# Kernel tuning notes

Measured on AMD Instinct MI355X. Metric: run time of the kernel, lower is better.

## Reference

```python
import jax, jax.numpy as jnp
import numpy as np
import math

EMBED_DIM = 256
N_HEAD = 8
N_LEVELS = 4
N_POINTS = 4
HEAD_DIM = EMBED_DIM // N_HEAD
TOTAL_POINTS = N_HEAD * N_LEVELS * N_POINTS
SPATIAL = np.array([[100, 100], [50, 50], [25, 25], [13, 13]], dtype=np.int32)
BS = 2
LEN_Q = int(SPATIAL.prod(1).sum())  # 13294, encoder self-attention
LEN_V = LEN_Q


def setup_inputs() -> dict:
    key = jax.random.key(0)
    ks = jax.random.split(key, 12)
    s = 1.0 / math.sqrt(EMBED_DIM)
    inp = {
        'query': jax.random.normal(ks[0], (BS, LEN_Q, EMBED_DIM), jnp.float32),
        'reference_points': jax.random.uniform(ks[1], (BS, LEN_Q, N_LEVELS, 2), jnp.float32),
        'value': jax.random.normal(ks[2], (BS, LEN_V, EMBED_DIM), jnp.float32),
        'value_spatial_shapes': jnp.asarray(SPATIAL),
        'W_value': jax.random.normal(ks[3], (EMBED_DIM, EMBED_DIM), jnp.float32) * s,
        'b_value': jnp.zeros((EMBED_DIM,), jnp.float32),
        'W_off': jax.random.normal(ks[4], (TOTAL_POINTS * 2, EMBED_DIM), jnp.float32) * 0.01,
        'b_off': jax.random.normal(ks[5], (TOTAL_POINTS * 2,), jnp.float32),
        'W_attn': jax.random.normal(ks[6], (TOTAL_POINTS, EMBED_DIM), jnp.float32) * s,
        'b_attn': jnp.zeros((TOTAL_POINTS,), jnp.float32),
        'W_out': jax.random.normal(ks[7], (EMBED_DIM, EMBED_DIM), jnp.float32) * s,
        'b_out': jnp.zeros((EMBED_DIM,), jnp.float32),
        'zeta': jnp.ones((1, 1, 1, HEAD_DIM), jnp.float32),  # search_type='embed'
    }
    return inp


def _grid_sample_bilinear(img, gx, gy):
    """img: [B,H,W,c]; gx,gy: [B,Q,P] normalized to [-1,1].
    align_corners=False, padding_mode='zeros' (matches F.grid_sample)."""
    B, H, W, c = img.shape
    x = (gx + 1.0) * (0.5 * W) - 0.5
    y = (gy + 1.0) * (0.5 * H) - 0.5
    x0 = jnp.floor(x)
    y0 = jnp.floor(y)
    wx = (x - x0)[..., None]
    wy = (y - y0)[..., None]
    flat = img.reshape(B, H * W, c)

    def gather(xi, yi):
        m = (xi >= 0) & (xi < W) & (yi >= 0) & (yi < H)
        xi_c = jnp.clip(xi, 0, W - 1).astype(jnp.int32)
        yi_c = jnp.clip(yi, 0, H - 1).astype(jnp.int32)
        idx = (yi_c * W + xi_c).reshape(B, -1, 1)
        v = jnp.take_along_axis(flat, idx, axis=1).reshape(B, *xi.shape[1:], c)
        return v * m[..., None]

    v00 = gather(x0, y0)
    v01 = gather(x0 + 1, y0)
    v10 = gather(x0, y0 + 1)
    v11 = gather(x0 + 1, y0 + 1)
    return (v00 * (1 - wx) * (1 - wy) + v01 * wx * (1 - wy)
            + v10 * (1 - wx) * wy + v11 * wx * wy)


def reference(query, reference_points, value, value_spatial_shapes,
              W_value, b_value, W_off, b_off, W_attn, b_attn, W_out, b_out, zeta):
    bs, Len_q, _ = query.shape
    Len_v = value.shape[1]
    shapes = np.asarray(value_spatial_shapes)  # static ints

    # value projection + sparse gate (zeta, not pruned/searched)
    v = value @ W_value.T + b_value
    v = v.reshape(bs, Len_v, N_HEAD, HEAD_DIM) * zeta  # [bs,Lv,h,c]

    # sampling offsets and attention weights from query
    off = (query @ W_off.T + b_off).reshape(bs, Len_q, N_HEAD, N_LEVELS, N_POINTS, 2)
    attn = (query @ W_attn.T + b_attn).reshape(bs, Len_q, N_HEAD, N_LEVELS * N_POINTS)
    attn = jax.nn.softmax(attn, axis=-1).reshape(bs, Len_q, N_HEAD, N_LEVELS, N_POINTS)

    # reference_points last dim == 2 branch
    normalizer = jnp.asarray(shapes[:, ::-1], jnp.float32).reshape(1, 1, 1, N_LEVELS, 1, 2)  # (W,H)
    loc = reference_points.reshape(bs, Len_q, 1, N_LEVELS, 1, 2) + off / normalizer
    grids = 2.0 * loc - 1.0  # [bs,Lq,h,L,P,2]

    B = bs * N_HEAD
    out = jnp.zeros((B, Len_q, HEAD_DIM), jnp.float32)
    start = 0
    for lvl in range(N_LEVELS):
        h, w = int(shapes[lvl, 0]), int(shapes[lvl, 1])
        # [bs, h*w, nh, c] -> [bs*nh, h, w, c]
        v_l = v[:, start:start + h * w].transpose(0, 2, 1, 3).reshape(B, h, w, HEAD_DIM)
        g = grids[:, :, :, lvl].transpose(0, 2, 1, 3, 4).reshape(B, Len_q, N_POINTS, 2)
        samp = _grid_sample_bilinear(v_l, g[..., 0], g[..., 1])  # [B,Lq,P,c]
        a_l = attn[:, :, :, lvl].transpose(0, 2, 1, 3).reshape(B, Len_q, N_POINTS)
        out = out + jnp.einsum('bqpc,bqp->bqc', samp, a_l)
        start += h * w

    out = out.reshape(bs, N_HEAD, Len_q, HEAD_DIM).transpose(0, 2, 1, 3).reshape(bs, Len_q, EMBED_DIM)
    return out @ W_out.T + b_out
```

## Files before the change

kernel.cpp:

```cpp
#include <hip/hip_runtime.h>


#define LQ    13294
#define NTOK  26588
#define NE    6806528

typedef unsigned short ushort_t;
typedef __attribute__((ext_vector_type(8))) short short8;
typedef __attribute__((ext_vector_type(4))) float float4_t;
typedef __attribute__((ext_vector_type(2))) unsigned int uint2_t;

__device__ __forceinline__ ushort_t f2b(float f) {
    unsigned int x = __float_as_uint(f);
    return (ushort_t)((x + 0x7fffu + ((x >> 16) & 1u)) >> 16);
}

__device__ __forceinline__ void gload16(const void* g, void* l) {
    __builtin_amdgcn_global_load_lds(
        (const __attribute__((address_space(1))) unsigned int*)g,
        (__attribute__((address_space(3))) unsigned int*)l, 16, 0, 0);
}

__device__ __forceinline__ void cvt_seg(const float* __restrict__ s,
                                        ushort_t* __restrict__ d,
                                        int n4, int gid, int stride) {
    const float4_t* s4 = (const float4_t*)s;
    for (int i = gid; i < n4; i += stride) {
        float4_t f = s4[i];
        ushort4 o;
        o.x = f2b(f.x); o.y = f2b(f.y); o.z = f2b(f.z); o.w = f2b(f.w);
        *(ushort4*)(d + (long)i * 4) = o;
    }
}

__global__ __launch_bounds__(256) void cvt_k(
    const float* q, const float* v, const float* Wv, const float* Wo,
    const float* Wa, const float* Wout,
    ushort_t* q_bf, ushort_t* v_bf, ushort_t* Wv_bf, ushort_t* WoWa_bf,
    ushort_t* Wout_bf)
{
    const int gid = blockIdx.x * 256 + threadIdx.x;
    const int stride = gridDim.x * 256;
    cvt_seg(q,    q_bf,            NE / 4,     gid, stride);
    cvt_seg(v,    v_bf,            NE / 4,     gid, stride);
    cvt_seg(Wv,   Wv_bf,           65536 / 4,  gid, stride);
    cvt_seg(Wo,   WoWa_bf,         65536 / 4,  gid, stride);
    cvt_seg(Wa,   WoWa_bf + 65536, 32768 / 4,  gid, stride);
    cvt_seg(Wout, Wout_bf,         65536 / 4,  gid, stride);
}

__device__ __forceinline__ void gemm_tile(
    const ushort_t* __restrict__ A,
    const ushort_t* __restrict__ W,
    int m0, int n0,
    ushort_t* As, ushort_t* Bs, float4_t acc[2][4])
{
    const int tid = threadIdx.x;
    const int w  = tid >> 6;
    const int ln = tid & 63;
    const int lr = ln >> 2;
    const int lc = (ln & 3) * 8;

    ushort_t* lA0 = As + (w * 2 + 0) * 512;
    ushort_t* lA1 = As + (w * 2 + 1) * 512;
    ushort_t* lB  = Bs + w * 512;
    const ushort_t* gA0 = A + (long)(m0 + w * 32 + lr) * 256 + lc;
    const ushort_t* gA1 = gA0 + 16 * 256;
    const ushort_t* gB  = W + (long)(n0 + w * 16 + lr) * 256 + lc;

    const int krow = (ln >> 4) * 8;
    const int fr   = ln & 15;

    for (int k0 = 0; k0 < 256; k0 += 32) {
        gload16(gA0 + k0, lA0);
        gload16(gA1 + k0, lA1);
        gload16(gB  + k0, lB);
        __syncthreads();

        short8 af[2], bfr[4];
        #pragma unroll
        for (int i = 0; i < 2; i++)
            af[i] = *(const short8*)(As + (w * 32 + i * 16 + fr) * 32 + krow);
        #pragma unroll
        for (int j = 0; j < 4; j++)
            bfr[j] = *(const short8*)(Bs + (j * 16 + fr) * 32 + krow);
        #pragma unroll
        for (int i = 0; i < 2; i++)
            #pragma unroll
            for (int j = 0; j < 4; j++)
                acc[i][j] = __builtin_amdgcn_mfma_f32_16x16x32_bf16(af[i], bfr[j], acc[i][j], 0, 0, 0);
        __syncthreads();
    }
}

__global__ __launch_bounds__(256) void gemm_fused_k(
    const ushort_t* __restrict__ q_bf, const ushort_t* __restrict__ v_bf,
    const ushort_t* __restrict__ Wv,   const ushort_t* __restrict__ WoWa,
    const float* __restrict__ b_value, const float* __restrict__ b_off,
    const float* __restrict__ b_attn,  const float* __restrict__ zeta,
    ushort_t* __restrict__ vproj, float* __restrict__ oa)
{
    __shared__ __align__(16) ushort_t As[128 * 32];
    __shared__ __align__(16) ushort_t Bs[64 * 32];

    const int z = blockIdx.z;
    const int bid = blockIdx.x;
    int x, y;
    if (z == 0) {
        if (bid >= 832) return;
        int id = (bid & 7) * 104 + (bid >> 3);
        x = id >> 2; y = id & 3;
    } else {
        int id = (bid & 7) * 156 + (bid >> 3);
        x = id / 6; y = id - x * 6;
    }
    const int m0 = x * 128;
    const int n0 = y * 64;

    float4_t acc[2][4] = {};
    gemm_tile(z ? q_bf : v_bf, z ? WoWa : Wv, m0, n0, As, Bs, acc);

    const int tid = threadIdx.x;
    const int w = tid >> 6, ln = tid & 63;
    const int col = ln & 15;
    const int rq  = (ln >> 4) * 4;
    #pragma unroll
    for (int j = 0; j < 4; j++) {
        int n = n0 + j * 16 + col;
        if (z == 0) {
            float bz = b_value[n];
            float zz = zeta[n & 31];
            #pragma unroll
            for (int i = 0; i < 2; i++) {
                #pragma unroll
                for (int r = 0; r < 4; r++) {
                    int m = m0 + w * 32 + i * 16 + rq + r;
                    if (m < NTOK) vproj[(long)m * 256 + n] = f2b((acc[i][j][r] + bz) * zz);
                }
            }
        } else {
            float bz = (n < 256) ? b_off[n] : b_attn[n - 256];
            #pragma unroll
            for (int i = 0; i < 2; i++) {
                #pragma unroll
                for (int r = 0; r < 4; r++) {
                    int m = m0 + w * 32 + i * 16 + rq + r;
                    if (m < NTOK) oa[(long)m * 384 + n] = acc[i][j][r] + bz;
                }
            }
        }
    }
}

__global__ __launch_bounds__(256) void gemm_out_k(
    const ushort_t* __restrict__ A,
    const ushort_t* __restrict__ W,
    const float* __restrict__ bias,
    float* __restrict__ C)
{
    __shared__ __align__(16) ushort_t As[128 * 32];
    __shared__ __align__(16) ushort_t Bs[64 * 32];

    const int bid = blockIdx.x;
    int id = (bid & 7) * 104 + (bid >> 3);
    const int m0 = (id >> 2) * 128;
    const int n0 = (id & 3) * 64;

    float4_t acc[2][4] = {};
    gemm_tile(A, W, m0, n0, As, Bs, acc);

    const int tid = threadIdx.x;
    const int w = tid >> 6, ln = tid & 63;
    const int col = ln & 15;
    const int rq  = (ln >> 4) * 4;
    #pragma unroll
    for (int j = 0; j < 4; j++) {
        int n = n0 + j * 16 + col;
        float bz = bias[n];
        #pragma unroll
        for (int i = 0; i < 2; i++) {
            #pragma unroll
            for (int r = 0; r < 4; r++) {
                int m = m0 + w * 32 + i * 16 + rq + r;
                if (m < NTOK) C[(long)m * 256 + n] = acc[i][j][r] + bz;
            }
        }
    }
}

__global__ __launch_bounds__(512) void sample_k(
    const float* __restrict__ refp,
    const ushort_t* __restrict__ v,
    const float* __restrict__ oa,
    ushort_t* __restrict__ outp)
{
    __shared__ int   p_ofs[512][4];
    __shared__ float p_w[512][4];
    const int tid = threadIdx.x;
    const int t0 = blockIdx.x * 4;

    {
        const int tok = tid >> 7, wt = tid & 127;
        const long t = t0 + tok;
        const int h = wt >> 4, pi = wt & 15;
        const int lvl = pi >> 2;
        const int Wi  = (lvl == 0) ? 100 : (lvl == 1) ? 50 : (lvl == 2) ? 25 : 13;
        const int st  = (lvl == 0) ? 0 : (lvl == 1) ? 10000 : (lvl == 2) ? 12500 : 13125;
        const float Wf = (float)Wi;

        float lg = oa[t * 384 + 256 + h * 16 + pi];
        float smax = lg;
        #pragma unroll
        for (int d = 1; d < 16; d <<= 1) smax = fmaxf(smax, __shfl_xor(smax, d, 64));
        float ex = __expf(lg - smax);
        float sm = ex;
        #pragma unroll
        for (int d = 1; d < 16; d <<= 1) sm += __shfl_xor(sm, d, 64);
        const float a = ex / sm;

        float ox = oa[t * 384 + h * 32 + pi * 2];
        float oy = oa[t * 384 + h * 32 + pi * 2 + 1];
        float rx = refp[t * 8 + lvl * 2];
        float ry = refp[t * 8 + lvl * 2 + 1];

        float x = rx * Wf + ox - 0.5f;
        float y = ry * Wf + oy - 0.5f;
        float xf = floorf(x), yf = floorf(y);
        float wx = x - xf, wy = y - yf;
        int x0 = (int)xf, y0 = (int)yf;

        float mx0 = ((unsigned)x0       < (unsigned)Wi) ? (1.f - wx) : 0.f;
        float mx1 = ((unsigned)(x0 + 1) < (unsigned)Wi) ? wx         : 0.f;
        float my0 = ((unsigned)y0       < (unsigned)Wi) ? (1.f - wy) * a : 0.f;
        float my1 = ((unsigned)(y0 + 1) < (unsigned)Wi) ? wy * a         : 0.f;
        int x0c = min(max(x0, 0), Wi - 1);
        int x1c = min(max(x0 + 1, 0), Wi - 1);
        int y0c = min(max(y0, 0), Wi - 1);
        int y1c = min(max(y0 + 1, 0), Wi - 1);

        int r0 = st + y0c * Wi, r1 = st + y1c * Wi;
        p_ofs[tid][0] = (r0 + x0c) << 9;
        p_ofs[tid][1] = (r0 + x1c) << 9;
        p_ofs[tid][2] = (r1 + x0c) << 9;
        p_ofs[tid][3] = (r1 + x1c) << 9;
        p_w[tid][0] = mx0 * my0;
        p_w[tid][1] = mx1 * my0;
        p_w[tid][2] = mx0 * my1;
        p_w[tid][3] = mx1 * my1;
    }
    __syncthreads();

    const int tok = tid >> 7, wt = tid & 127;
    const long t = t0 + tok;
    const int b = (t >= LQ) ? 1 : 0;
    const int h = wt >> 4, s = (wt >> 3) & 1, g = wt & 7;
    const char* vb = (const char*)(v + ((long)b * LQ) * 256 + h * 32 + g * 4);
    const int base = tok * 128 + h * 16 + s * 8;
    float4_t acc = {0.f, 0.f, 0.f, 0.f};

    #pragma unroll 4
    for (int p = 0; p < 8; p++) {
        int4     o  = *(const int4*)p_ofs[base + p];
        float4_t w4 = *(const float4_t*)p_w[base + p];
        uint2_t u00 = *(const uint2_t*)(vb + o.x);
        uint2_t u01 = *(const uint2_t*)(vb + o.y);
        uint2_t u10 = *(const uint2_t*)(vb + o.z);
        uint2_t u11 = *(const uint2_t*)(vb + o.w);
        acc[0] += w4.x * __uint_as_float(u00.x << 16)
                + w4.y * __uint_as_float(u01.x << 16)
                + w4.z * __uint_as_float(u10.x << 16)
                + w4.w * __uint_as_float(u11.x << 16);
        acc[1] += w4.x * __uint_as_float(u00.x & 0xffff0000u)
                + w4.y * __uint_as_float(u01.x & 0xffff0000u)
                + w4.z * __uint_as_float(u10.x & 0xffff0000u)
                + w4.w * __uint_as_float(u11.x & 0xffff0000u);
        acc[2] += w4.x * __uint_as_float(u00.y << 16)
                + w4.y * __uint_as_float(u01.y << 16)
                + w4.z * __uint_as_float(u10.y << 16)
                + w4.w * __uint_as_float(u11.y << 16);
        acc[3] += w4.x * __uint_as_float(u00.y & 0xffff0000u)
                + w4.y * __uint_as_float(u01.y & 0xffff0000u)
                + w4.z * __uint_as_float(u10.y & 0xffff0000u)
                + w4.w * __uint_as_float(u11.y & 0xffff0000u);
    }

    acc.x += __shfl_down(acc.x, 8, 64);
    acc.y += __shfl_down(acc.y, 8, 64);
    acc.z += __shfl_down(acc.z, 8, 64);
    acc.w += __shfl_down(acc.w, 8, 64);

    if (s == 0) {
        ushort4 o;
        o.x = f2b(acc.x); o.y = f2b(acc.y); o.z = f2b(acc.z); o.w = f2b(acc.w);
        *(ushort4*)(outp + t * 256 + h * 32 + g * 4) = o;
    }
}

extern "C" void kernel_launch(void* const* d_in, const int* in_sizes, int n_in,
                              void* d_out, int out_size, void* d_ws, size_t ws_size,
                              hipStream_t stream)
{
    char* ws = (char*)d_ws;
    ushort_t* vproj   = (ushort_t*)ws;
    float*    oa      = (float*)(ws + (long)NE * 2);
    ushort_t* q_bf    = (ushort_t*)(ws + (long)NE * 2 + (long)NTOK * 1536);
    ushort_t* outpre  = q_bf;
    ushort_t* v_bf    = q_bf + NE;
    ushort_t* Wv_bf   = v_bf + NE;
    ushort_t* WoWa_bf = Wv_bf + 65536;
    ushort_t* Wout_bf = WoWa_bf + 98304;

    cvt_k<<<1024, 256, 0, stream>>>(
        (const float*)d_in[0], (const float*)d_in[2], (const float*)d_in[4],
        (const float*)d_in[6], (const float*)d_in[8], (const float*)d_in[10],
        q_bf, v_bf, Wv_bf, WoWa_bf, Wout_bf);

    gemm_fused_k<<<dim3(1248, 1, 2), 256, 0, stream>>>(
        q_bf, v_bf, Wv_bf, WoWa_bf,
        (const float*)d_in[5], (const float*)d_in[7], (const float*)d_in[9],
        (const float*)d_in[12], vproj, oa);

    sample_k<<<6647, 512, 0, stream>>>(
        (const float*)d_in[1], vproj, oa, outpre);

    gemm_out_k<<<832, 256, 0, stream>>>(
        outpre, Wout_bf, (const float*)d_in[11], (float*)d_out);
}
```

Baseline: 224.5 us.

## Head-major value layout, 16-byte gathers, and double-buffered GEMM tiles with preloaded weights

The value projection is now stored head-major ([head][token][32]), so each bilinear corner of one head is a contiguous 64-byte row. The sampler gathers 16 bytes per lane instead of 8, processes 8 tokens per block with padded shared-memory indexing, and halves the grid. The GEMM tile preloads the whole 64x256 weight slice into LDS and double-buffers the A tiles, which removes one barrier per k-step. In exchange, LDS per block grows substantially, which may reduce occupancy.

```diff
diff --git a/kernel.cpp b/kernel.cpp
--- a/kernel.cpp
+++ b/kernel.cpp
@@ -7,8 +7,8 @@
 
 typedef unsigned short ushort_t;
 typedef __attribute__((ext_vector_type(8))) short short8;
+typedef __attribute__((ext_vector_type(8))) unsigned short ushort8_t;
 typedef __attribute__((ext_vector_type(4))) float float4_t;
-typedef __attribute__((ext_vector_type(2))) unsigned int uint2_t;
 
 __device__ __forceinline__ ushort_t f2b(float f) {
     unsigned int x = __float_as_uint(f);
@@ -53,7 +53,7 @@
     const ushort_t* __restrict__ A,
     const ushort_t* __restrict__ W,
     int m0, int n0,
-    ushort_t* As, ushort_t* Bs, float4_t acc[2][4])
+    ushort_t* Asb, ushort_t* Bs, float4_t acc[2][4])
 {
     const int tid = threadIdx.x;
     const int w  = tid >> 6;
@@ -61,29 +61,35 @@
     const int lr = ln >> 2;
     const int lc = (ln & 3) * 8;
 
-    ushort_t* lA0 = As + (w * 2 + 0) * 512;
-    ushort_t* lA1 = As + (w * 2 + 1) * 512;
-    ushort_t* lB  = Bs + w * 512;
+    const ushort_t* gB = W + (long)(n0 + w * 16 + lr) * 256 + lc;
+    #pragma unroll
+    for (int kt = 0; kt < 8; kt++)
+        gload16(gB + kt * 32, Bs + kt * 2048 + w * 512);
+
     const ushort_t* gA0 = A + (long)(m0 + w * 32 + lr) * 256 + lc;
     const ushort_t* gA1 = gA0 + 16 * 256;
-    const ushort_t* gB  = W + (long)(n0 + w * 16 + lr) * 256 + lc;
+    gload16(gA0, Asb + (w * 2 + 0) * 512);
+    gload16(gA1, Asb + (w * 2 + 1) * 512);
+    __syncthreads();
 
     const int krow = (ln >> 4) * 8;
     const int fr   = ln & 15;
 
-    for (int k0 = 0; k0 < 256; k0 += 32) {
-        gload16(gA0 + k0, lA0);
-        gload16(gA1 + k0, lA1);
-        gload16(gB  + k0, lB);
-        __syncthreads();
-
+    #pragma unroll
+    for (int kt = 0; kt < 8; kt++) {
+        const int cur = (kt & 1) * 4096;
+        if (kt < 7) {
+            const int nxt = 4096 - cur;
+            gload16(gA0 + (kt + 1) * 32, Asb + nxt + (w * 2 + 0) * 512);
+            gload16(gA1 + (kt + 1) * 32, Asb + nxt + (w * 2 + 1) * 512);
+        }
         short8 af[2], bfr[4];
         #pragma unroll
         for (int i = 0; i < 2; i++)
-            af[i] = *(const short8*)(As + (w * 32 + i * 16 + fr) * 32 + krow);
+            af[i] = *(const short8*)(Asb + cur + (w * 32 + i * 16 + fr) * 32 + krow);
         #pragma unroll
         for (int j = 0; j < 4; j++)
-            bfr[j] = *(const short8*)(Bs + (j * 16 + fr) * 32 + krow);
+            bfr[j] = *(const short8*)(Bs + kt * 2048 + (j * 16 + fr) * 32 + krow);
         #pragma unroll
         for (int i = 0; i < 2; i++)
             #pragma unroll
@@ -100,8 +106,8 @@
     const float* __restrict__ b_attn,  const float* __restrict__ zeta,
     ushort_t* __restrict__ vproj, float* __restrict__ oa)
 {
-    __shared__ __align__(16) ushort_t As[128 * 32];
-    __shared__ __align__(16) ushort_t Bs[64 * 32];
+    __shared__ __align__(16) ushort_t Asb[8192];
+    __shared__ __align__(16) ushort_t Bs[16384];
 
     const int z = blockIdx.z;
     const int bid = blockIdx.x;
@@ -118,7 +124,7 @@
     const int n0 = y * 64;
 
     float4_t acc[2][4] = {};
-    gemm_tile(z ? q_bf : v_bf, z ? WoWa : Wv, m0, n0, As, Bs, acc);
+    gemm_tile(z ? q_bf : v_bf, z ? WoWa : Wv, m0, n0, Asb, Bs, acc);
 
     const int tid = threadIdx.x;
     const int w = tid >> 6, ln = tid & 63;
@@ -130,12 +136,14 @@
         if (z == 0) {
             float bz = b_value[n];
             float zz = zeta[n & 31];
+            long hbase = (long)(n >> 5) * NTOK;
             #pragma unroll
             for (int i = 0; i < 2; i++) {
                 #pragma unroll
                 for (int r = 0; r < 4; r++) {
                     int m = m0 + w * 32 + i * 16 + rq + r;
-                    if (m < NTOK) vproj[(long)m * 256 + n] = f2b((acc[i][j][r] + bz) * zz);
+                    if (m < NTOK)
+                        vproj[(hbase + m) * 32 + (n & 31)] = f2b((acc[i][j][r] + bz) * zz);
                 }
             }
         } else {
@@ -158,8 +166,8 @@
     const float* __restrict__ bias,
     float* __restrict__ C)
 {
-    __shared__ __align__(16) ushort_t As[128 * 32];
-    __shared__ __align__(16) ushort_t Bs[64 * 32];
+    __shared__ __align__(16) ushort_t Asb[8192];
+    __shared__ __align__(16) ushort_t Bs[16384];
 
     const int bid = blockIdx.x;
     int id = (bid & 7) * 104 + (bid >> 3);
@@ -167,7 +175,7 @@
     const int n0 = (id & 3) * 64;
 
     float4_t acc[2][4] = {};
-    gemm_tile(A, W, m0, n0, As, Bs, acc);
+    gemm_tile(A, W, m0, n0, Asb, Bs, acc);
 
     const int tid = threadIdx.x;
     const int w = tid >> 6, ln = tid & 63;
@@ -194,105 +202,118 @@
     const float* __restrict__ oa,
     ushort_t* __restrict__ outp)
 {
-    __shared__ int   p_ofs[512][4];
-    __shared__ float p_w[512][4];
+    __shared__ __align__(16) int   p_ofs[1152][4];
+    __shared__ __align__(16) float p_w[1152][4];
     const int tid = threadIdx.x;
-    const int t0 = blockIdx.x * 4;
-
-    {
-        const int tok = tid >> 7, wt = tid & 127;
-        const long t = t0 + tok;
-        const int h = wt >> 4, pi = wt & 15;
-        const int lvl = pi >> 2;
-        const int Wi  = (lvl == 0) ? 100 : (lvl == 1) ? 50 : (lvl == 2) ? 25 : 13;
-        const int st  = (lvl == 0) ? 0 : (lvl == 1) ? 10000 : (lvl == 2) ? 12500 : 13125;
-        const float Wf = (float)Wi;
-
-        float lg = oa[t * 384 + 256 + h * 16 + pi];
-        float smax = lg;
-        #pragma unroll
-        for (int d = 1; d < 16; d <<= 1) smax = fmaxf(smax, __shfl_xor(smax, d, 64));
-        float ex = __expf(lg - smax);
-        float sm = ex;
-        #pragma unroll
-        for (int d = 1; d < 16; d <<= 1) sm += __shfl_xor(sm, d, 64);
-        const float a = ex / sm;
-
-        float ox = oa[t * 384 + h * 32 + pi * 2];
-        float oy = oa[t * 384 + h * 32 + pi * 2 + 1];
-        float rx = refp[t * 8 + lvl * 2];
-        float ry = refp[t * 8 + lvl * 2 + 1];
-
-        float x = rx * Wf + ox - 0.5f;
-        float y = ry * Wf + oy - 0.5f;
-        float xf = floorf(x), yf = floorf(y);
-        float wx = x - xf, wy = y - yf;
-        int x0 = (int)xf, y0 = (int)yf;
-
-        float mx0 = ((unsigned)x0       < (unsigned)Wi) ? (1.f - wx) : 0.f;
-        float mx1 = ((unsigned)(x0 + 1) < (unsigned)Wi) ? wx         : 0.f;
-        float my0 = ((unsigned)y0       < (unsigned)Wi) ? (1.f - wy) * a : 0.f;
-        float my1 = ((unsigned)(y0 + 1) < (unsigned)Wi) ? wy * a         : 0.f;
-        int x0c = min(max(x0, 0), Wi - 1);
-        int x1c = min(max(x0 + 1, 0), Wi - 1);
-        int y0c = min(max(y0, 0), Wi - 1);
-        int y1c = min(max(y0 + 1, 0), Wi - 1);
-
-        int r0 = st + y0c * Wi, r1 = st + y1c * Wi;
-        p_ofs[tid][0] = (r0 + x0c) << 9;
-        p_ofs[tid][1] = (r0 + x1c) << 9;
-        p_ofs[tid][2] = (r1 + x0c) << 9;
-        p_ofs[tid][3] = (r1 + x1c) << 9;
-        p_w[tid][0] = mx0 * my0;
-        p_w[tid][1] = mx1 * my0;
-        p_w[tid][2] = mx0 * my1;
-        p_w[tid][3] = mx1 * my1;
+    const int tok = tid >> 6;
+    const int ln  = tid & 63;
+    const long t  = (long)blockIdx.x * 8 + tok;
+    const bool valid = (t < NTOK);
+    const int b = (t >= LQ) ? 1 : 0;
+
+    if (valid) {
+        #pragma unroll
+        for (int half = 0; half < 2; half++) {
+            const int h  = (ln >> 4) + half * 4;
+            const int pi = ln & 15;
+            const int lvl = pi >> 2;
+            const int Wi  = (lvl == 0) ? 100 : (lvl == 1) ? 50 : (lvl == 2) ? 25 : 13;
+            const int st  = (lvl == 0) ? 0 : (lvl == 1) ? 10000 : (lvl == 2) ? 12500 : 13125;
+            const float Wf = (float)Wi;
+
+            float lg = oa[t * 384 + 256 + h * 16 + pi];
+            float smax = lg;
+            #pragma unroll
+            for (int d = 1; d < 16; d <<= 1) smax = fmaxf(smax, __shfl_xor(smax, d, 64));
+            float ex = __expf(lg - smax);
+            float sm = ex;
+            #pragma unroll
+            for (int d = 1; d < 16; d <<= 1) sm += __shfl_xor(sm, d, 64);
+            const float a = ex / sm;
+
+            float ox = oa[t * 384 + h * 32 + pi * 2];
+            float oy = oa[t * 384 + h * 32 + pi * 2 + 1];
+            float rx = refp[t * 8 + lvl * 2];
+            float ry = refp[t * 8 + lvl * 2 + 1];
+
+            float x = rx * Wf + ox - 0.5f;
+            float y = ry * Wf + oy - 0.5f;
+            float xf = floorf(x), yf = floorf(y);
+            float wx = x - xf, wy = y - yf;
+            int x0 = (int)xf, y0 = (int)yf;
+
+            float mx0 = ((unsigned)x0       < (unsigned)Wi) ? (1.f - wx) : 0.f;
+            float mx1 = ((unsigned)(x0 + 1) < (unsigned)Wi) ? wx         : 0.f;
+            float my0 = ((unsigned)y0       < (unsigned)Wi) ? (1.f - wy) * a : 0.f;
+            float my1 = ((unsigned)(y0 + 1) < (unsigned)Wi) ? wy * a         : 0.f;
+            int x0c = min(max(x0, 0), Wi - 1);
+            int x1c = min(max(x0 + 1, 0), Wi - 1);
+            int y0c = min(max(y0, 0), Wi - 1);
+            int y1c = min(max(y0 + 1, 0), Wi - 1);
+
+            const int hb = h * NTOK + b * LQ + st;
+            int r0 = hb + y0c * Wi, r1 = hb + y1c * Wi;
+            const int u  = tok * 128 + half * 64 + ln;
+            const int su = u + (u >> 3);
+            p_ofs[su][0] = (r0 + x0c) << 6;
+            p_ofs[su][1] = (r0 + x1c) << 6;
+            p_ofs[su][2] = (r1 + x0c) << 6;
+            p_ofs[su][3] = (r1 + x1c) << 6;
+            p_w[su][0] = mx0 * my0;
+            p_w[su][1] = mx1 * my0;
+            p_w[su][2] = mx0 * my1;
+            p_w[su][3] = mx1 * my1;
+        }
     }
     __syncthreads();
 
-    const int tok = tid >> 7, wt = tid & 127;
-    const long t = t0 + tok;
-    const int b = (t >= LQ) ? 1 : 0;
-    const int h = wt >> 4, s = (wt >> 3) & 1, g = wt & 7;
-    const char* vb = (const char*)(v + ((long)b * LQ) * 256 + h * 32 + g * 4);
+    if (!valid) return;
+
+    const int h = ln >> 3, s = (ln >> 2) & 1, g = ln & 3;
+    const char* vb = (const char*)v;
+    const unsigned go = g * 16;
     const int base = tok * 128 + h * 16 + s * 8;
-    float4_t acc = {0.f, 0.f, 0.f, 0.f};
-
-    #pragma unroll 4
+    const int skb  = base + (base >> 3);
+    float4_t accA = {0.f, 0.f, 0.f, 0.f};
+    float4_t accB = {0.f, 0.f, 0.f, 0.f};
+
+    #pragma unroll 2
     for (int p = 0; p < 8; p++) {
-        int4     o  = *(const int4*)p_ofs[base + p];
-        float4_t w4 = *(const float4_t*)p_w[base + p];
-        uint2_t u00 = *(const uint2_t*)(vb + o.x);
-        uint2_t u01 = *(const uint2_t*)(vb + o.y);
-        uint2_t u10 = *(const uint2_t*)(vb + o.z);
-        uint2_t u11 = *(const uint2_t*)(vb + o.w);
-        acc[0] += w4.x * __uint_as_float(u00.x << 16)
-                + w4.y * __uint_as_float(u01.x << 16)
-                + w4.z * __uint_as_float(u10.x << 16)
-                + w4.w * __uint_as_float(u11.x << 16);
-        acc[1] += w4.x * __uint_as_float(u00.x & 0xffff0000u)
-                + w4.y * __uint_as_float(u01.x & 0xffff0000u)
-                + w4.z * __uint_as_float(u10.x & 0xffff0000u)
-                + w4.w * __uint_as_float(u11.x & 0xffff0000u);
-        acc[2] += w4.x * __uint_as_float(u00.y << 16)
-                + w4.y * __uint_as_float(u01.y << 16)
-                + w4.z * __uint_as_float(u10.y << 16)
-                + w4.w * __uint_as_float(u11.y << 16);
-        acc[3] += w4.x * __uint_as_float(u00.y & 0xffff0000u)
-                + w4.y * __uint_as_float(u01.y & 0xffff0000u)
-                + w4.z * __uint_as_float(u10.y & 0xffff0000u)
-                + w4.w * __uint_as_float(u11.y & 0xffff0000u);
-    }
-
-    acc.x += __shfl_down(acc.x, 8, 64);
-    acc.y += __shfl_down(acc.y, 8, 64);
-    acc.z += __shfl_down(acc.z, 8, 64);
-    acc.w += __shfl_down(acc.w, 8, 64);
-
-    if (s == 0) {
-        ushort4 o;
-        o.x = f2b(acc.x); o.y = f2b(acc.y); o.z = f2b(acc.z); o.w = f2b(acc.w);
-        *(ushort4*)(outp + t * 256 + h * 32 + g * 4) = o;
+        int4     o  = *(const int4*)p_ofs[skb + p];
+        float4_t w4 = *(const float4_t*)p_w[skb + p];
+        uint4 u00 = *(const uint4*)(vb + (unsigned)(o.x + go));
+        uint4 u01 = *(const uint4*)(vb + (unsigned)(o.y + go));
+        uint4 u10 = *(const uint4*)(vb + (unsigned)(o.z + go));
+        uint4 u11 = *(const uint4*)(vb + (unsigned)(o.w + go));
+        #define ACC8(U, WGT) \
+            accA[0] += (WGT) * __uint_as_float((U).x << 16); \
+            accA[1] += (WGT) * __uint_as_float((U).x & 0xffff0000u); \
+            accA[2] += (WGT) * __uint_as_float((U).y << 16); \
+            accA[3] += (WGT) * __uint_as_float((U).y & 0xffff0000u); \
+            accB[0] += (WGT) * __uint_as_float((U).z << 16); \
+            accB[1] += (WGT) * __uint_as_float((U).z & 0xffff0000u); \
+            accB[2] += (WGT) * __uint_as_float((U).w << 16); \
+            accB[3] += (WGT) * __uint_as_float((U).w & 0xffff0000u);
+        ACC8(u00, w4.x)
+        ACC8(u01, w4.y)
+        ACC8(u10, w4.z)
+        ACC8(u11, w4.w)
+        #undef ACC8
+    }
+
+    #pragma unroll
+    for (int c = 0; c < 4; c++) {
+        accA[c] += __shfl_down(accA[c], 4, 64);
+        accB[c] += __shfl_down(accB[c], 4, 64);
+    }
+
+    if ((ln & 4) == 0) {
+        ushort8_t o8;
+        o8[0] = f2b(accA[0]); o8[1] = f2b(accA[1]);
+        o8[2] = f2b(accA[2]); o8[3] = f2b(accA[3]);
+        o8[4] = f2b(accB[0]); o8[5] = f2b(accB[1]);
+        o8[6] = f2b(accB[2]); o8[7] = f2b(accB[3]);
+        *(ushort8_t*)(outp + t * 256 + h * 32 + g * 8) = o8;
     }
 }
 
@@ -320,7 +341,7 @@
         (const float*)d_in[5], (const float*)d_in[7], (const float*)d_in[9],
         (const float*)d_in[12], vproj, oa);
 
-    sample_k<<<6647, 512, 0, stream>>>(
+    sample_k<<<3324, 512, 0, stream>>>(
         (const float*)d_in[1], vproj, oa, outpre);
 
     gemm_out_k<<<832, 256, 0, stream>>>(
```

Measured after the change: 224.5 us. Within noise of the previous version (+0.0%).
